# Kernel tuning notes

Hardware: AMD Instinct MI355X
Metric: run time of the kernel (lower is better)

The kernel has to match this reference:

```python
import jax, jax.numpy as jnp
import numpy as np

T, NC, NQ = 16, 32, 32
H, W, C = 128, 128, 1
DW, DR, DZ = 256, 256, 128
LABEL_DIM, Y_DIM = 2, 2
NHEADS = 8
NFEAT = int(DW * np.log(DW))  # performer default nb_features = int(d*ln d) = 1419


def setup_inputs() -> dict:
    key = jax.random.key(0)
    ks = iter(jax.random.split(key, 48))
    def nrm(shape, scale=0.02):
        return jax.random.normal(next(ks), shape, dtype=jnp.float32) * scale
    z = lambda *s: jnp.zeros(s, jnp.float32)
    return {
        'batch_train_images': jax.random.normal(next(ks), (T, NC, C, H, W), jnp.float32),
        'label_train': jax.random.normal(next(ks), (T, NC, LABEL_DIM), jnp.float32),
        'batch_test_images': jax.random.normal(next(ks), (T, NQ, C, H, W), jnp.float32),
        'conv1_w': nrm((32, C, 3, 3), 0.1), 'conv1_b': z(32),
        'conv2_w': nrm((48, 32, 3, 3), 0.05), 'conv2_b': z(48),
        'conv3_w': nrm((64, 48, 3, 3), 0.05), 'conv3_b': z(64),
        'enc_lw': nrm((DW, 4096)), 'enc_lb': z(DW),
        'ty_w': nrm((DW // 4, LABEL_DIM)), 'ty_b': z(DW // 4),
        'er_w1': nrm((DR, DW + DW // 4), 0.05), 'er_b1': z(DR),
        'er_w2': nrm((DR, DR), 0.05), 'er_b2': z(DR),
        'er_w3': nrm((DR, DR), 0.05), 'er_b3': z(DR),
        'wq': nrm((NHEADS, DW, DW), 0.05), 'wq_b': z(NHEADS, DW),
        'wk': nrm((NHEADS, DW, DW), 0.05), 'wk_b': z(NHEADS, DW),
        'wv': nrm((NHEADS, DW, DW), 0.05), 'wv_b': z(NHEADS, DW),
        'wo_w': nrm((DW, NHEADS * DW), 0.02), 'wo_b': z(DW),
        'rz_w': nrm((DZ, DR), 0.05), 'rz_b': z(DZ),
        'd0_w1': nrm((100, DW + DZ), 0.05), 'd0_b1': z(100),
        'd0_w2': nrm((100, 100), 0.05), 'd0_b2': z(100),
        'd0_w3': nrm((Y_DIM, 100), 0.05), 'd0_b3': z(Y_DIM),
        'proj': jax.random.normal(next(ks), (NFEAT, DW), jnp.float32),
    }


def _conv(x, w, b, stride):
    y = jax.lax.conv_general_dilated(x, w, (stride, stride), [(1, 1), (1, 1)],
                                     dimension_numbers=('NCHW', 'OIHW', 'NCHW'))
    return y + b[None, :, None, None]


def _maxpool2(x):
    return jax.lax.reduce_window(x, -jnp.inf, jax.lax.max, (1, 1, 2, 2), (1, 1, 2, 2), 'VALID')


def _encode(x, c1w, c1b, c2w, c2b, c3w, c3b, lw, lb):
    # BBBEncoder (mean weights): 128->64->32->pool16->8, 64ch, flatten 4096 -> DW
    x = jax.nn.relu(_conv(x, c1w, c1b, 2))
    x = jax.nn.relu(_conv(x, c2w, c2b, 2))
    x = _maxpool2(x)
    x = jax.nn.relu(_conv(x, c3w, c3b, 2))
    x = x.reshape(x.shape[0], -1)  # [B, 4096], NCHW order matches torch view
    return x @ lw.T + lb


def _softmax_kernel(x, proj, is_query):
    # performer softmax-kernel random features
    dn = x.shape[-1] ** -0.25
    ratio = proj.shape[0] ** -0.5
    xn = x * dn
    xd = jnp.einsum('bhnd,fd->bhnf', xn, proj)
    diag = 0.5 * jnp.sum(xn * xn, axis=-1, keepdims=True)
    if is_query:
        m = jnp.max(xd, axis=-1, keepdims=True)
    else:
        m = jnp.max(xd, axis=(-1, -2), keepdims=True)
    return ratio * (jnp.exp(xd - diag - jax.lax.stop_gradient(m)) + 1e-4)


def _forward(batch_train_images, label_train, batch_test_images,
             conv1_w, conv1_b, conv2_w, conv2_b, conv3_w, conv3_b, enc_lw, enc_lb,
             ty_w, ty_b, er_w1, er_b1, er_w2, er_b2, er_w3, er_b3,
             wq, wq_b, wk, wk_b, wv, wv_b, wo_w, wo_b, rz_w, rz_b,
             d0_w1, d0_b1, d0_w2, d0_b2, d0_w3, d0_b3, proj):
    enc = lambda im: _encode(im, conv1_w, conv1_b, conv2_w, conv2_b, conv3_w, conv3_b, enc_lw, enc_lb)
    x_qry = enc(batch_test_images.reshape(-1, C, H, W)).reshape(T, NQ, DW)
    x_ctx = enc(batch_train_images.reshape(-1, C, H, W)).reshape(T, NC, DW)
    ly = label_train @ ty_w.T + ty_b
    x = jnp.concatenate([x_ctx, ly], axis=2)  # [T, NC, DW + DW//4]
    h = jax.nn.relu(x @ er_w1.T + er_b1)
    h = jax.nn.relu(h @ er_w2.T + er_b2)
    rs = h @ er_w3.T + er_b3  # [T, NC, DR]
    # per-head projections (batched over the 8 heads)
    k_all = jnp.einsum('bnd,hed->bhne', x_ctx, wk) + wk_b[None, :, None, :]
    v_all = jnp.einsum('bnd,hed->bhne', rs, wv) + wv_b[None, :, None, :]
    q_all = jnp.einsum('bnd,hed->bhne', x_qry, wq) + wq_b[None, :, None, :]
    qp = _softmax_kernel(q_all, proj, True)   # [T, H, NQ, F]
    kp = _softmax_kernel(k_all, proj, False)  # [T, H, NC, F]
    d_inv = 1.0 / jnp.einsum('bhnf,bhf->bhn', qp, kp.sum(axis=2))
    ctx_mat = jnp.einsum('bhnf,bhne->bhfe', kp, v_all)
    outs = jnp.einsum('bhnf,bhfe->bhne', qp, ctx_mat) * d_inv[..., None]
    outs = outs.transpose(0, 2, 3, 1).reshape(T, NQ, -1)  # permute(0,2,3,1).view
    rep = outs @ wo_w.T + wo_b
    zz = rep @ rz_w.T + rz_b  # [T, NQ, DZ]
    xz = jnp.concatenate([x_qry, zz], axis=-1)
    h = jax.nn.relu(xz @ d0_w1.T + d0_b1)
    h = jax.nn.relu(h @ d0_w2.T + d0_b2)
    return jnp.tanh(h @ d0_w3.T + d0_b3)  # pr_y_mu [T, NQ, Y_DIM]


def reference(batch_train_images, label_train, batch_test_images,
              conv1_w, conv1_b, conv2_w, conv2_b, conv3_w, conv3_b, enc_lw, enc_lb,
              ty_w, ty_b, er_w1, er_b1, er_w2, er_b2, er_w3, er_b3,
              wq, wq_b, wk, wk_b, wv, wv_b, wo_w, wo_b, rz_w, rz_b,
              d0_w1, d0_b1, d0_w2, d0_b2, d0_w3, d0_b3, proj):
    pr_y_mu = _forward(batch_train_images, label_train, batch_test_images,
                       conv1_w, conv1_b, conv2_w, conv2_b, conv3_w, conv3_b, enc_lw, enc_lb,
                       ty_w, ty_b, er_w1, er_b1, er_w2, er_b2, er_w3, er_b3,
                       wq, wq_b, wk, wk_b, wv, wv_b, wo_w, wo_b, rz_w, rz_b,
                       d0_w1, d0_b1, d0_w2, d0_b2, d0_w3, d0_b3, proj)
    kl = jnp.float32(0.0)  # deterministic (mean-weight) BBB encoder -> KL constant
    return (pr_y_mu, kl)
```

## Files before the change

### kernel.cpp

```cpp
#include <hip/hip_runtime.h>
#include <math.h>

#define F_FEAT 1419
static constexpr float DN    = 0.25f;

typedef short short8 __attribute__((ext_vector_type(8)));
typedef float f32x4  __attribute__((ext_vector_type(4)));

static constexpr long OFF_XDQ  = 0;
static constexpr long OFF_XDK  = 5812224;
static constexpr long U_WQH = 0;
static constexpr long U_WQL = 524288;
static constexpr long U_WKH = 1048576;
static constexpr long U_WKL = 1572864;
static constexpr long U_WVH = 2097152;
static constexpr long U_WVL = 2621440;
static constexpr long OFF_ENCT = 4000000;
static constexpr long OFF_REPT = 6200000;
static constexpr long U_PH  = 23248896;
static constexpr long U_PL  = 23625728;
static constexpr long U_XCH = 24002560;
static constexpr long U_XCL = 24264704;
static constexpr long U_RSH = 24526848;
static constexpr long U_RSL = 24657920;
static constexpr long U_C3H = 25165824;
static constexpr long U_C3L = 29360128;
static constexpr long U_WOH = 25165824;
static constexpr long U_WOL = 25690112;
static constexpr long BASE     = 16777216;
static constexpr long OFF_XCTX = BASE + 0;
static constexpr long OFF_XQRY = BASE + 131072;
static constexpr long OFF_XCAT = BASE + 262144;
static constexpr long OFF_H1   = BASE + 425984;
static constexpr long OFF_H2   = BASE + 557056;
static constexpr long OFF_RS   = BASE + 688128;
static constexpr long U_QH  = (BASE + 819200) * 2;
static constexpr long U_QL  = U_QH + 1048576;
static constexpr long U_KH  = (BASE + 1867776) * 2;
static constexpr long U_KL  = U_KH + 1048576;
static constexpr long OFF_VA   = BASE + 2916352;
static constexpr long OFF_AW1  = BASE + 3964928;
static constexpr long U_ELH = (BASE + 3977344) * 2;
static constexpr long U_ELL = U_ELH + 1048576;
static constexpr long U_REPH = U_ELH;
static constexpr long U_REPL = U_ELL;
static constexpr long OFF_REP  = BASE + 5025920;
static constexpr long OFF_XZ   = BASE + 5156992;
static constexpr long OFF_DH1  = BASE + 5353600;
static constexpr long OFF_DH2  = BASE + 5404800;
static constexpr long OFF_MD   = BASE + 5456000;
static constexpr long OFF_AW   = 22233216;
static constexpr long OFF_AW3  = 22240128;

__device__ inline unsigned short f2bf(float f) {
    unsigned int x = __float_as_uint(f);
    unsigned int r = x + 0x7fffu + ((x >> 16) & 1u);
    return (unsigned short)(r >> 16);
}
__device__ inline float bf2f(unsigned short h) {
    return __uint_as_float((unsigned int)h << 16);
}
__device__ inline unsigned int cvtpk(float a, float b) {
    unsigned int r;
    asm("v_cvt_pk_bf16_f32 %0, %1, %2" : "=v"(r) : "v"(a), "v"(b));
    return r;
}

static constexpr int NA1 = 13824;
static constexpr int NA2 = NA1 + 1024;
static constexpr int NA3 = NA2 + 73728;
static constexpr int NA4 = NA3 + 1048576;

__global__ void k_wprepA(const float* __restrict__ w2, const float* __restrict__ w1,
                         const float* __restrict__ w3, const float* __restrict__ elw,
                         unsigned short* __restrict__ Aw, unsigned short* __restrict__ Aw1,
                         unsigned short* __restrict__ Aw3,
                         unsigned short* __restrict__ ELh, unsigned short* __restrict__ ELl)
{
    int i = blockIdx.x * 256 + threadIdx.x;
    if (i < NA1) {
        int ic  = i & 31;
        int m16 = (i >> 5) & 15;
        int emt = i >> 9;
        int mt  = emt % 3, e = emt / 3;
        Aw[i] = f2bf(w2[((mt * 16 + m16) * 32 + ic) * 9 + e]);
    } else if (i < NA2) {
        int j = i - NA1;
        int k = j & 31, m = (j >> 5) & 15, mt = j >> 9;
        Aw1[j] = (k < 9) ? f2bf(w1[(mt * 16 + m) * 9 + k]) : (unsigned short)0;
    } else if (i < NA3) {
        int j = i - NA2;
        int k  = j & 63;
        int m  = (j >> 6) & 15;
        int hl = (j >> 10) & 1;
        int mt = (j >> 11) & 3;
        int e  = j >> 13;
        unsigned short v = 0;
        if (k < 48) {
            float w = w3[((mt * 16 + m) * 48 + k) * 9 + e];
            unsigned short hi = f2bf(w);
            v = hl == 0 ? hi : f2bf(w - bf2f(hi));
        }
        Aw3[j] = v;
    } else if (i < NA4) {
        int j = i - NA3;
        float v = elw[j];
        unsigned short h = f2bf(v);
        ELh[j] = h; ELl[j] = f2bf(v - bf2f(h));
    }
}

static constexpr int NB1 = 376832;
static constexpr int NB2 = NB1 + 1572864;

__global__ void k_wprepB(const float* __restrict__ proj,
                         const float* __restrict__ wq, const float* __restrict__ wk,
                         const float* __restrict__ wv,
                         unsigned short* __restrict__ Ph, unsigned short* __restrict__ Pl,
                         unsigned short* __restrict__ Wqkv)
{
    int i = blockIdx.x * 256 + threadIdx.x;
    if (i < NB1) {
        float v = (i < 363264) ? proj[i] : 0.f;
        unsigned short h = f2bf(v);
        Ph[i] = h; Pl[i] = f2bf(v - bf2f(h));
    } else if (i < NB2) {
        int j = i - NB1;
        int y = j / 524288, jj = j % 524288;
        const float* s = (y == 0) ? wq : (y == 1) ? wk : wv;
        float v = s[jj];
        unsigned short h = f2bf(v);
        Wqkv[(long)y * 1048576 + jj] = h;
        Wqkv[(long)y * 1048576 + 524288 + jj] = f2bf(v - bf2f(h));
    }
}

#define TP 136
__launch_bounds__(256)
__global__ void k_conv12m(const float* __restrict__ train, const float* __restrict__ test,
                          const float* __restrict__ b1,
                          const unsigned short* __restrict__ Aw,
                          const unsigned short* __restrict__ Aw1,
                          const float* __restrict__ b2,
                          unsigned short* __restrict__ pool_out)
{
    const int g   = blockIdx.x;
    const int img = blockIdx.y;
    const float* in = (img < 512) ? (train + (long)img * 16384)
                                  : (test  + (long)(img - 512) * 16384);

    __shared__ unsigned short ring[9 * 66 * 40];
    __shared__ unsigned short tile[19 * TP];

    const int t = threadIdx.x;

    for (int i = t; i < 9 * 40; i += 256) {
        int sl = i / 40, icp = i % 40;
        ring[(sl * 66 + 0) * 40 + icp] = 0;
    }
    if (g == 0)
        for (int i = t; i < 66 * 40; i += 256) ring[i] = 0;
    if (t < 19) *(unsigned int*)&tile[t * TP + 2] = 0u;

    {
        const float4 z4 = make_float4(0.f, 0.f, 0.f, 0.f);
        for (int u = t; u < 19 * 32; u += 256) {
            int row = u >> 5, k = u & 31;
            int r2 = 16 * g - 3 + row;
            float4 v = (r2 >= 0) ? *(const float4*)(in + r2 * 128 + k * 4) : z4;
            uint2 d;
            d.x = cvtpk(v.x, v.y);
            d.y = cvtpk(v.z, v.w);
            *(uint2*)&tile[row * TP + 4 + k * 4] = d;
        }
    }
    __syncthreads();

    const int w    = t >> 6;
    const int lane = t & 63;
    const int cn   = lane & 15;
    const int quad = lane >> 4;

    short8 a1f0 = *(const short8*)&Aw1[(0 * 16 + cn) * 32 + quad * 8];
    short8 a1f1 = *(const short8*)&Aw1[(16 + cn) * 32 + quad * 8];
    float4 bsa = *(const float4*)&b1[quad * 4];
    float4 bsb = *(const float4*)&b1[16 + quad * 4];

    const int px2 = w * 16 + cn;
    const int tb  = 2 * px2 + 2;
    auto do_slice = [&](int sl) {
        const int rb = 2 * sl * TP + tb;
        uint4 pk = make_uint4(0u, 0u, 0u, 0u);
        if (quad == 0) {
            unsigned int w00 = *(const unsigned int*)&tile[rb];
            unsigned int w10 = *(const unsigned int*)&tile[rb + 2];
            unsigned int w01 = *(const unsigned int*)&tile[rb + TP];
            unsigned int w11 = *(const unsigned int*)&tile[rb + TP + 2];
            unsigned int w02 = *(const unsigned int*)&tile[rb + 2 * TP];
            unsigned int w12 = *(const unsigned int*)&tile[rb + 2 * TP + 2];
            pk.x = (w00 >> 16) | (w10 << 16);
            pk.y = (w10 >> 16) | (w01 & 0xffff0000u);
            pk.z = w11;
            pk.w = (w02 >> 16) | (w12 << 16);
        } else if (quad == 1) {
            pk.x = (*(const unsigned int*)&tile[rb + 2 * TP + 2]) >> 16;
        }
        short8 bfr = *(const short8*)&pk;
        f32x4 z = (f32x4){0.f, 0.f, 0.f, 0.f};
        f32x4 c0 = __builtin_amdgcn_mfma_f32_16x16x32_bf16(a1f0, bfr, z, 0, 0, 0);
        f32x4 c1 = __builtin_amdgcn_mfma_f32_16x16x32_bf16(a1f1, bfr, z, 0, 0, 0);
        uint2 u0, u1;
        u0.x = cvtpk(fmaxf(c0[0] + bsa.x, 0.f), fmaxf(c0[1] + bsa.y, 0.f));
        u0.y = cvtpk(fmaxf(c0[2] + bsa.z, 0.f), fmaxf(c0[3] + bsa.w, 0.f));
        u1.x = cvtpk(fmaxf(c1[0] + bsb.x, 0.f), fmaxf(c1[1] + bsb.y, 0.f));
        u1.y = cvtpk(fmaxf(c1[2] + bsb.z, 0.f), fmaxf(c1[3] + bsb.w, 0.f));
        *(uint2*)&ring[(sl * 66 + px2 + 1) * 40 + quad * 4]      = u0;
        *(uint2*)&ring[(sl * 66 + px2 + 1) * 40 + 16 + quad * 4] = u1;
    };
    if (g > 0) do_slice(0);
    #pragma unroll
    for (int sl = 1; sl < 9; sl++) do_slice(sl);

    short8 ca0 = *(const short8*)&Aw[((0 * 3 + 0) * 16 + cn) * 32 + quad * 8];
    short8 ca1 = *(const short8*)&Aw[((0 * 3 + 1) * 16 + cn) * 32 + quad * 8];
    short8 ca2 = *(const short8*)&Aw[((0 * 3 + 2) * 16 + cn) * 32 + quad * 8];
    __syncthreads();

    const int pr = w >> 1, xh = w & 1;
    f32x4 acc[3][2];
    #pragma unroll
    for (int mt = 0; mt < 3; mt++) {
        acc[mt][0] = (f32x4){0.f, 0.f, 0.f, 0.f};
        acc[mt][1] = (f32x4){0.f, 0.f, 0.f, 0.f};
    }

    #pragma unroll
    for (int e = 0; e < 9; e++) {
        int dy = e / 3, dx = e - 3 * dy;
        int c  = 2 * (xh * 16 + cn) + dx;
        int s0 = 4 * pr + dy;
        short8 b0  = *(const short8*)&ring[(s0 * 66 + c) * 40 + quad * 8];
        short8 b1f = *(const short8*)&ring[((s0 + 2) * 66 + c) * 40 + quad * 8];
        short8 na0, na1, na2;
        if (e < 8) {
            na0 = *(const short8*)&Aw[(((e + 1) * 3 + 0) * 16 + cn) * 32 + quad * 8];
            na1 = *(const short8*)&Aw[(((e + 1) * 3 + 1) * 16 + cn) * 32 + quad * 8];
            na2 = *(const short8*)&Aw[(((e + 1) * 3 + 2) * 16 + cn) * 32 + quad * 8];
        }
        acc[0][0] = __builtin_amdgcn_mfma_f32_16x16x32_bf16(ca0, b0,  acc[0][0], 0, 0, 0);
        acc[1][0] = __builtin_amdgcn_mfma_f32_16x16x32_bf16(ca1, b0,  acc[1][0], 0, 0, 0);
        acc[2][0] = __builtin_amdgcn_mfma_f32_16x16x32_bf16(ca2, b0,  acc[2][0], 0, 0, 0);
        acc[0][1] = __builtin_amdgcn_mfma_f32_16x16x32_bf16(ca0, b1f, acc[0][1], 0, 0, 0);
        acc[1][1] = __builtin_amdgcn_mfma_f32_16x16x32_bf16(ca1, b1f, acc[1][1], 0, 0, 0);
        acc[2][1] = __builtin_amdgcn_mfma_f32_16x16x32_bf16(ca2, b1f, acc[2][1], 0, 0, 0);
        if (e < 8) { ca0 = na0; ca1 = na1; ca2 = na2; }
    }

    {
        const int prow = 2 * g + pr;
        const int ppx  = xh * 8 + (cn >> 1);
        unsigned short* pb = pool_out + ((long)img * 256 + prow * 16 + ppx) * 96
                           + ((cn & 1) ? 48 : 0);
        #pragma unroll
        for (int mt = 0; mt < 3; mt++) {
            float4 bv = *(const float4*)&b2[mt * 16 + quad * 4];
            float m0, m1, m2, m3;
            {
                float v;
                v = fmaxf(fmaxf(acc[mt][0][0] + bv.x, acc[mt][1][0] + bv.x), 0.f);
                m0 = fmaxf(v, __shfl_xor(v, 1));
                v = fmaxf(fmaxf(acc[mt][0][1] + bv.y, acc[mt][1][1] + bv.y), 0.f);
                m1 = fmaxf(v, __shfl_xor(v, 1));
                v = fmaxf(fmaxf(acc[mt][0][2] + bv.z, acc[mt][1][2] + bv.z), 0.f);
                m2 = fmaxf(v, __shfl_xor(v, 1));
                v = fmaxf(fmaxf(acc[mt][0][3] + bv.w, acc[mt][1][3] + bv.w), 0.f);
                m3 = fmaxf(v, __shfl_xor(v, 1));
            }
            uint2 hv;
            hv.x = cvtpk(m0, m1);
            hv.y = cvtpk(m2, m3);
            uint2 sv = hv;
            if (cn & 1) {
                float d0 = m0 - bf2f((unsigned short)(hv.x & 0xffffu));
                float d1 = m1 - bf2f((unsigned short)(hv.x >> 16));
                float d2 = m2 - bf2f((unsigned short)(hv.y & 0xffffu));
                float d3 = m3 - bf2f((unsigned short)(hv.y >> 16));
                sv.x = cvtpk(d0, d1);
                sv.y = cvtpk(d2, d3);
            }
            *(uint2*)&pb[mt * 16 + quad * 4] = sv;
        }
    }
}

#define C3PITCH 104
__launch_bounds__(512)
__global__ void k_conv3m(const unsigned short* __restrict__ pool,
                         const unsigned short* __restrict__ Aw3,
                         const float* __restrict__ b3,
                         unsigned short* __restrict__ C3h, unsigned short* __restrict__ C3l)
{
    const int img = blockIdx.x;
    __shared__ unsigned short s_in[30120];
    const int t = threadIdx.x;

    uint4* s4 = (uint4*)s_in;
    const uint4 zz = make_uint4(0, 0, 0, 0);
    for (int i = t; i < 3765; i += 512) s4[i] = zz;
    __syncthreads();
    {
        int p = t >> 1, half = t & 1;
        const uint4* src = (const uint4*)(pool + ((long)img * 256 + p) * 96 + half * 48);
        int r = p >> 4, c = p & 15;
        uint4* dst = (uint4*)(s_in + ((r + 1) * 17 + (c + 1)) * C3PITCH + half * 48);
        #pragma unroll
        for (int j = 0; j < 6; j++) dst[j] = src[j];
    }
    __syncthreads();

    const int w = t >> 6, lane = t & 63;
    const int n = lane & 15, quad = lane >> 4;
    const int mt = w >> 1, ntb = (w & 1) * 2;

    f32x4 acc[2];
    acc[0] = (f32x4){0.f, 0.f, 0.f, 0.f};
    acc[1] = (f32x4){0.f, 0.f, 0.f, 0.f};

    for (int e = 0; e < 9; e++) {
        int dy = e / 3, dx = e - 3 * dy;
        const unsigned short* A0 = Aw3 + (long)(((e * 4 + mt) * 2 + 0) * 16 + n) * 64 + quad * 8;
        const unsigned short* A1 = Aw3 + (long)(((e * 4 + mt) * 2 + 1) * 16 + n) * 64 + quad * 8;
        short8 ah0 = *(const short8*)(A0);
        short8 ah1 = *(const short8*)(A0 + 32);
        short8 al0 = *(const short8*)(A1);
        short8 al1 = *(const short8*)(A1 + 32);
        #pragma unroll
        for (int j = 0; j < 2; j++) {
            int p = (ntb + j) * 16 + n;
            int y = p >> 3, x = p & 7;
            const unsigned short* Bp = s_in + ((2 * y + dy) * 17 + (2 * x + dx)) * C3PITCH + quad * 8;
            short8 bh0 = *(const short8*)(Bp);
            short8 bh1 = *(const short8*)(Bp + 32);
            short8 bl0 = *(const short8*)(Bp + 48);
            short8 bl1 = *(const short8*)(Bp + 48 + 32);
            acc[j] = __builtin_amdgcn_mfma_f32_16x16x32_bf16(ah0, bh0, acc[j], 0, 0, 0);
            acc[j] = __builtin_amdgcn_mfma_f32_16x16x32_bf16(ah1, bh1, acc[j], 0, 0, 0);
            acc[j] = __builtin_amdgcn_mfma_f32_16x16x32_bf16(ah0, bl0, acc[j], 0, 0, 0);
            acc[j] = __builtin_amdgcn_mfma_f32_16x16x32_bf16(ah1, bl1, acc[j], 0, 0, 0);
            acc[j] = __builtin_amdgcn_mfma_f32_16x16x32_bf16(al0, bh0, acc[j], 0, 0, 0);
            acc[j] = __builtin_amdgcn_mfma_f32_16x16x32_bf16(al1, bh1, acc[j], 0, 0, 0);
        }
    }

    unsigned short* oh = C3h + (long)img * 4096;
    unsigned short* ol = C3l + (long)img * 4096;
    #pragma unroll
    for (int reg = 0; reg < 4; reg++) {
        int oc = mt * 16 + quad * 4 + reg;
        float bias = b3[oc];
        #pragma unroll
        for (int j = 0; j < 2; j++) {
            int p = (ntb + j) * 16 + n;
            float v = fmaxf(acc[j][reg] + bias, 0.f);
            unsigned short h = f2bf(v);
            oh[oc * 64 + p] = h;
            ol[oc * 64 + p] = f2bf(v - bf2f(h));
        }
    }
}

template<int OUTMODE>
__launch_bounds__(256)
__global__ void mgemm(const unsigned short* __restrict__ Xh0, const unsigned short* __restrict__ Xl0,
                      const unsigned short* __restrict__ Wph, const unsigned short* __restrict__ Wpl,
                      const float* __restrict__ Bb, float* __restrict__ Yf,
                      unsigned short* __restrict__ Yh, unsigned short* __restrict__ Yl,
                      int M, int N, int K, int ldY, float scale,
                      long sX, long sW, long sB, long sY, int kChunk)
{
    const int z = blockIdx.z;
    const unsigned short* Xh = Xh0 + (OUTMODE == 3 ? 0 : (long)z * sX);
    const unsigned short* Xl = Xl0 + (OUTMODE == 3 ? 0 : (long)z * sX);
    const unsigned short* Wh = Wph + (OUTMODE == 3 ? 0 : (long)z * sW);
    const unsigned short* Wl = Wpl + (OUTMODE == 3 ? 0 : (long)z * sW);
    const float* B = Bb ? (Bb + (OUTMODE == 3 ? 0 : (long)z * sB)) : nullptr;
    int k0 = 0, k1 = K;
    if (OUTMODE == 3) { k0 = z * kChunk; k1 = min(K, k0 + kChunk); }

    __shared__ unsigned short sAh[64 * 40], sAl[64 * 40], sBh[64 * 40], sBl[64 * 40];

    const int t = threadIdx.x;
    const int m0 = blockIdx.y * 64, n0 = blockIdx.x * 64;
    const int r = t >> 2, kq = (t & 3) * 8;

    const int w = t >> 6, lane = t & 63;
    const int wm = (w & 1) * 32, wn = (w >> 1) * 32;
    const int cn = lane & 15, quad = lane >> 4;

    f32x4 acc[2][2];
    acc[0][0] = acc[0][1] = acc[1][0] = acc[1][1] = (f32x4){0.f, 0.f, 0.f, 0.f};

    for (int kb = k0; kb < k1; kb += 32) {
        *(uint4*)&sAh[r * 40 + kq] = *(const uint4*)&Xh[(long)(m0 + r) * K + kb + kq];
        *(uint4*)&sAl[r * 40 + kq] = *(const uint4*)&Xl[(long)(m0 + r) * K + kb + kq];
        *(uint4*)&sBh[r * 40 + kq] = *(const uint4*)&Wh[(long)(n0 + r) * K + kb + kq];
        *(uint4*)&sBl[r * 40 + kq] = *(const uint4*)&Wl[(long)(n0 + r) * K + kb + kq];
        __syncthreads();
        short8 axh[2], axl[2], bxh[2], bxl[2];
        #pragma unroll
        for (int i = 0; i < 2; i++) {
            axh[i] = *(const short8*)&sAh[(wm + i * 16 + cn) * 40 + quad * 8];
            axl[i] = *(const short8*)&sAl[(wm + i * 16 + cn) * 40 + quad * 8];
            bxh[i] = *(const short8*)&sBh[(wn + i * 16 + cn) * 40 + quad * 8];
            bxl[i] = *(const short8*)&sBl[(wn + i * 16 + cn) * 40 + quad * 8];
        }
        #pragma unroll
        for (int i = 0; i < 2; i++)
            #pragma unroll
            for (int j = 0; j < 2; j++) {
                acc[i][j] = __builtin_amdgcn_mfma_f32_16x16x32_bf16(axh[i], bxh[j], acc[i][j], 0, 0, 0);
                acc[i][j] = __builtin_amdgcn_mfma_f32_16x16x32_bf16(axh[i], bxl[j], acc[i][j], 0, 0, 0);
                acc[i][j] = __builtin_amdgcn_mfma_f32_16x16x32_bf16(axl[i], bxh[j], acc[i][j], 0, 0, 0);
            }
        __syncthreads();
    }

    #pragma unroll
    for (int i = 0; i < 2; i++) {
        #pragma unroll
        for (int reg = 0; reg < 4; reg++) {
            int row = m0 + wm + i * 16 + quad * 4 + reg;
            #pragma unroll
            for (int j = 0; j < 2; j++) {
                int col = n0 + wn + j * 16 + cn;
                if (col >= N) continue;
                float v = acc[i][j][reg] * scale;
                if (OUTMODE == 3) {
                    (Yf + (long)z * sY)[(long)row * ldY + col] = v;
                } else if (OUTMODE == 0) {
                    if (B) v += B[col];
                    (Yf + (long)z * sY)[(long)row * ldY + col] = v;
                } else {
                    if (B) v += B[col];
                    unsigned short h = f2bf(v);
                    (Yh + (long)z * sY)[(long)row * ldY + col] = h;
                    (Yl + (long)z * sY)[(long)row * ldY + col] = f2bf(v - bf2f(h));
                }
            }
        }
    }
}

__global__ void k_red_enc(const float* __restrict__ tmp, const float* __restrict__ elb,
                          float* __restrict__ x_ctx, unsigned short* __restrict__ XCh,
                          unsigned short* __restrict__ XCl, float* __restrict__ xcat,
                          const float* __restrict__ label, const float* __restrict__ tyw,
                          const float* __restrict__ tyb,
                          const float* __restrict__ wow, unsigned short* __restrict__ WOh,
                          unsigned short* __restrict__ WOl)
{
    int b = blockIdx.x;
    int tt = threadIdx.x;
    if (b < 1024) {
        int i = b * 256 + tt;
        int r = i >> 8, c = i & 255;
        float v = elb[c];
        #pragma unroll
        for (int z = 0; z < 8; z++) v += tmp[(long)z * 262144 + i];
        x_ctx[i] = v;
        unsigned short h = f2bf(v);
        XCh[i] = h; XCl[i] = f2bf(v - bf2f(h));
        if (r < 512) xcat[r * 320 + c] = v;
    } else if (b < 1152) {
        int i = (b - 1024) * 256 + tt;
        int r = i >> 6, e = i & 63;
        xcat[r * 320 + 256 + e] = tyb[e] + label[r * 2] * tyw[e * 2] + label[r * 2 + 1] * tyw[e * 2 + 1];
    } else {
        int i = (b - 1152) * 256 + tt;
        float v = wow[i];
        unsigned short h = f2bf(v);
        WOh[i] = h; WOl[i] = f2bf(v - bf2f(h));
    }
}

__global__ void k_red_rep(const float* __restrict__ tmp, const float* __restrict__ wob,
                          float* __restrict__ rep,
                          const float* __restrict__ xq, float* __restrict__ xz)
{
    int b = blockIdx.x;
    int tt = threadIdx.x;
    if (b < 512) {
        int i = b * 256 + tt;
        int c = i & 255;
        float v = wob[c];
        #pragma unroll
        for (int z = 0; z < 4; z++) v += tmp[(long)z * 131072 + i];
        rep[i] = v;
    } else {
        int i = (b - 512) * 256 + tt;
        int r = i >> 8, c = i & 255;
        xz[r * 384 + c] = xq[i];
    }
}

template<int BM, int BN, int BK, int ACT, bool FIN, bool WP>
__launch_bounds__(256)
__global__ void gemm_k(const float* __restrict__ X, const float* __restrict__ W,
                       const float* __restrict__ B, float* __restrict__ Y,
                       int M, int N, int K, int ldY,
                       unsigned short* __restrict__ Ph2, unsigned short* __restrict__ Pl2)
{
    __shared__ float As[BK][BM + 4];
    __shared__ float Bs[BK][BN + 4];
    const int t = threadIdx.x;
    const int tx = t & 15, ty = t >> 4;
    const int m0 = blockIdx.y * BM, n0 = blockIdx.x * BN;
    float acc[2][2] = {{0.f, 0.f}, {0.f, 0.f}};

    for (int kb = 0; kb < K; kb += BK) {
        for (int i = t; i < BM * BK; i += 256) {
            int rr = i / BK, c = i % BK;
            int mm = m0 + rr, kk = kb + c;
            As[c][rr] = (mm < M && kk < K) ? X[(long)mm * K + kk] : 0.f;
        }
        for (int i = t; i < BN * BK; i += 256) {
            int rr = i / BK, c = i % BK;
            int nn = n0 + rr, kk = kb + c;
            Bs[c][rr] = (nn < N && kk < K) ? W[(long)nn * K + kk] : 0.f;
        }
        __syncthreads();
        #pragma unroll
        for (int kk = 0; kk < BK; kk++) {
            float2 a2 = *(const float2*)&As[kk][ty * 2];
            float2 b2 = *(const float2*)&Bs[kk][tx * 2];
            acc[0][0] += a2.x * b2.x; acc[0][1] += a2.x * b2.y;
            acc[1][0] += a2.y * b2.x; acc[1][1] += a2.y * b2.y;
        }
        __syncthreads();
    }

    #pragma unroll
    for (int i = 0; i < 2; i++) {
        int mm = m0 + ty * 2 + i;
        if (mm >= M) continue;
        #pragma unroll
        for (int j = 0; j < 2; j++) {
            int nn = n0 + tx * 2 + j;
            if (nn >= N) continue;
            float v = acc[i][j] + (B ? B[nn] : 0.f);
            if (ACT == 1) v = fmaxf(v, 0.f);
            if (ACT == 2) v = tanhf(v);
            Y[(long)mm * ldY + nn] = v;
            if (WP) {
                unsigned short h = f2bf(v);
                Ph2[(long)mm * ldY + nn] = h;
                Pl2[(long)mm * ldY + nn] = f2bf(v - bf2f(h));
            }
        }
    }
    if (FIN && t == 0 && blockIdx.x == 0 && blockIdx.y == 0) Y[1024] = 0.f;
}

__launch_bounds__(256)
__global__ void k_maxdiag(const float* __restrict__ xdq, const float* __restrict__ xdk,
                          const unsigned short* __restrict__ Qh, const unsigned short* __restrict__ Ql,
                          const unsigned short* __restrict__ Kh, const unsigned short* __restrict__ Kl,
                          float* __restrict__ dq, float* __restrict__ mq,
                          float* __restrict__ dk, float* __restrict__ mk)
{
    __shared__ float red[8];
    const int bx = blockIdx.x;
    const int t = threadIdx.x;

    if (bx < 4096) {
        const int tok = bx;
        float v = bf2f(Qh[(long)tok * 256 + t]) + bf2f(Ql[(long)tok * 256 + t]);
        float s = v * v;
        for (int d = 1; d < 64; d <<= 1) s += __shfl_xor(s, d);
        if ((t & 63) == 0) red[t >> 6] = s;

        float m = -1e30f;
        #pragma unroll
        for (int j = 0; j < 6; j++) {
            int f = t + j * 256;
            if (f < F_FEAT) m = fmaxf(m, xdq[(long)tok * F_FEAT + f]);
        }
        for (int d = 1; d < 64; d <<= 1) m = fmaxf(m, __shfl_xor(m, d));
        if ((t & 63) == 0) red[4 + (t >> 6)] = m;
        __syncthreads();
        if (t == 0) {
            dq[tok] = (red[0] + red[1] + red[2] + red[3]) * (1.f / 32.f);
            mq[tok] = fmaxf(fmaxf(red[4], red[5]), fmaxf(red[6], red[7]));
        }
    } else {
        const int kb = bx - 4096;
        const long tok0 = (long)kb * 32;
        const int row = t >> 3, j = t & 7;

        float s = 0.f;
        const unsigned short* ph = Kh + (tok0 + row) * 256 + j * 32;
        const unsigned short* pl = Kl + (tok0 + row) * 256 + j * 32;
        for (int q = 0; q < 32; q++) { float v = bf2f(ph[q]) + bf2f(pl[q]); s += v * v; }
        s += __shfl_xor(s, 1); s += __shfl_xor(s, 2); s += __shfl_xor(s, 4);
        if (j == 0) dk[tok0 + row] = s * (1.f / 32.f);

        const float* base = xdk + tok0 * F_FEAT;
        float m = -1e30f;
        for (int i = t; i < 32 * F_FEAT; i += 256) m = fmaxf(m, base[i]);
        for (int d = 1; d < 64; d <<= 1) m = fmaxf(m, __shfl_xor(m, d));
        if ((t & 63) == 0) red[t >> 6] = m;
        __syncthreads();
        if (t == 0) mk[kb] = fmaxf(fmaxf(red[0], red[1]), fmaxf(red[2], red[3]));
    }
}

__launch_bounds__(256)
__global__ void k_attn(const float* __restrict__ qp, const float* __restrict__ kp,
                       const float* __restrict__ va,
                       const float* __restrict__ dq, const float* __restrict__ mq,
                       const float* __restrict__ dk, const float* __restrict__ mk,
                       unsigned short* __restrict__ REPh, unsigned short* __restrict__ REPl)
{
    const int tt = blockIdx.x;
    const int h  = blockIdx.y;
    const long row0 = ((long)h * 16 + tt) * 32;
    const int kb = h * 16 + tt;

    __shared__ float s_q[32][68];
    __shared__ float s_k[32][68];
    __shared__ float s_A[32][33];
    __shared__ float s_di[32];
    __shared__ float s_v[32 * 256];
    __shared__ float s_cq[32], s_ck[32];

    const int t = threadIdx.x;
    const int n = t >> 3;
    const int mq_ = (t & 7) * 4;

    if (t < 32) {
        s_cq[t] = dq[row0 + t] + mq[row0 + t];
        s_ck[t] = dk[row0 + t] + mk[kb];
    }
    __syncthreads();

    float acc[4] = {0, 0, 0, 0};
    for (int fc = 0; fc < F_FEAT; fc += 64) {
        for (int i = t; i < 2048; i += 256) {
            int rr = i >> 6, ff = i & 63;
            int fg = fc + ff;
            if (fg < F_FEAT) {
                s_q[rr][ff] = expf(qp[(row0 + rr) * F_FEAT + fg] - s_cq[rr]) + 1e-4f;
                s_k[rr][ff] = expf(kp[(row0 + rr) * F_FEAT + fg] - s_ck[rr]) + 1e-4f;
            } else {
                s_q[rr][ff] = 0.f;
                s_k[rr][ff] = 0.f;
            }
        }
        __syncthreads();
        #pragma unroll 8
        for (int ff = 0; ff < 64; ff++) {
            float a = s_q[n][ff];
            #pragma unroll
            for (int j = 0; j < 4; j++) acc[j] += a * s_k[mq_ + j][ff];
        }
        __syncthreads();
    }

    float rsum = acc[0] + acc[1] + acc[2] + acc[3];
    rsum += __shfl_xor(rsum, 1);
    rsum += __shfl_xor(rsum, 2);
    rsum += __shfl_xor(rsum, 4);
    #pragma unroll
    for (int j = 0; j < 4; j++) s_A[n][mq_ + j] = acc[j];
    if ((t & 7) == 0) s_di[n] = 1.f / rsum;
    for (int i = t; i < 8192; i += 256) s_v[i] = va[row0 * 256 + i];
    __syncthreads();

    const int e0 = t & 7;
    float out[32];
    #pragma unroll
    for (int j = 0; j < 32; j++) out[j] = 0.f;
    for (int m = 0; m < 32; m++) {
        float a = s_A[n][m];
        #pragma unroll
        for (int j = 0; j < 32; j++) out[j] += a * s_v[m * 256 + e0 + 8 * j];
    }
    float di = s_di[n];
    unsigned short* dsth = REPh + ((long)tt * 32 + n) * 2048;
    unsigned short* dstl = REPl + ((long)tt * 32 + n) * 2048;
    #pragma unroll
    for (int j = 0; j < 32; j++) {
        int e = e0 + 8 * j;
        float val = out[j] * di;
        unsigned short hh = f2bf(val);
        dsth[e * 8 + h] = hh;
        dstl[e * 8 + h] = f2bf(val - bf2f(hh));
    }
}

extern "C" void kernel_launch(void* const* d_in, const int* in_sizes, int n_in,
                              void* d_out, int out_size, void* d_ws, size_t ws_size,
                              hipStream_t stream)
{
    const float* train  = (const float*)d_in[0];
    const float* label  = (const float*)d_in[1];
    const float* test   = (const float*)d_in[2];
    const float* c1w = (const float*)d_in[3];  const float* c1b = (const float*)d_in[4];
    const float* c2w = (const float*)d_in[5];  const float* c2b = (const float*)d_in[6];
    const float* c3w = (const float*)d_in[7];  const float* c3b = (const float*)d_in[8];
    const float* elw = (const float*)d_in[9];  const float* elb = (const float*)d_in[10];
    const float* tyw = (const float*)d_in[11]; const float* tyb = (const float*)d_in[12];
    const float* ew1 = (const float*)d_in[13]; const float* eb1 = (const float*)d_in[14];
    const float* ew2 = (const float*)d_in[15]; const float* eb2 = (const float*)d_in[16];
    const float* ew3 = (const float*)d_in[17]; const float* eb3 = (const float*)d_in[18];
    const float* wq  = (const float*)d_in[19]; const float* wqb = (const float*)d_in[20];
    const float* wk  = (const float*)d_in[21]; const float* wkb = (const float*)d_in[22];
    const float* wv  = (const float*)d_in[23]; const float* wvb = (const float*)d_in[24];
    const float* wow = (const float*)d_in[25]; const float* wob = (const float*)d_in[26];
    const float* rzw = (const float*)d_in[27]; const float* rzb = (const float*)d_in[28];
    const float* dw1 = (const float*)d_in[29]; const float* db1 = (const float*)d_in[30];
    const float* dw2 = (const float*)d_in[31]; const float* db2 = (const float*)d_in[32];
    const float* dw3 = (const float*)d_in[33]; const float* db3 = (const float*)d_in[34];
    const float* proj= (const float*)d_in[35];

    float* wsf = (float*)d_ws;
    unsigned short* usw = (unsigned short*)d_ws;
    float* out = (float*)d_out;

    unsigned short* A_pool = usw;
    float* x_ctx  = wsf + OFF_XCTX;
    float* x_qry  = wsf + OFF_XQRY;
    float* xcat   = wsf + OFF_XCAT;
    float* h1     = wsf + OFF_H1;
    float* h2     = wsf + OFF_H2;
    float* rs     = wsf + OFF_RS;
    float* v_all  = wsf + OFF_VA;
    float* rep    = wsf + OFF_REP;
    float* xz     = wsf + OFF_XZ;
    float* dh1    = wsf + OFF_DH1;
    float* dh2    = wsf + OFF_DH2;
    float* xd_q   = wsf + OFF_XDQ;
    float* xd_k   = wsf + OFF_XDK;
    float* enc_t  = wsf + OFF_ENCT;
    float* rep_t  = wsf + OFF_REPT;
    float* dqv    = wsf + OFF_MD;
    float* mqv    = wsf + OFF_MD + 4096;
    float* dkv    = wsf + OFF_MD + 8192;
    float* mkv    = wsf + OFF_MD + 12288;
    unsigned short* Aw  = (unsigned short*)(wsf + OFF_AW);
    unsigned short* Aw3 = (unsigned short*)(wsf + OFF_AW3);
    unsigned short* Aw1 = (unsigned short*)(wsf + OFF_AW1);

    unsigned short* Wqkv = usw + U_WQH;
    unsigned short* WQh = usw + U_WQH; unsigned short* WQl = usw + U_WQL;
    unsigned short* WKh = usw + U_WKH; unsigned short* WKl = usw + U_WKL;
    unsigned short* WVh = usw + U_WVH; unsigned short* WVl = usw + U_WVL;
    unsigned short* Ph  = usw + U_PH;  unsigned short* Pl  = usw + U_PL;
    unsigned short* XCh = usw + U_XCH; unsigned short* XCl = usw + U_XCL;
    unsigned short* RSh = usw + U_RSH; unsigned short* RSl = usw + U_RSL;
    unsigned short* C3h = usw + U_C3H; unsigned short* C3l = usw + U_C3L;
    unsigned short* Qh  = usw + U_QH;  unsigned short* Ql  = usw + U_QL;
    unsigned short* Kh  = usw + U_KH;  unsigned short* Kl  = usw + U_KL;
    unsigned short* ELh = usw + U_ELH; unsigned short* ELl = usw + U_ELL;
    unsigned short* WOh = usw + U_WOH; unsigned short* WOl = usw + U_WOL;
    unsigned short* REPh= usw + U_REPH;unsigned short* REPl= usw + U_REPL;

    k_wprepA<<<4442, 256, 0, stream>>>(c2w, c1w, c3w, elw, Aw, Aw1, Aw3, ELh, ELl);

    k_conv12m<<<dim3(8, 1024), 256, 0, stream>>>(train, test, c1b, Aw, Aw1, c2b, A_pool);
    k_conv3m<<<1024, 512, 0, stream>>>(A_pool, Aw3, c3b, C3h, C3l);

    k_wprepB<<<7616, 256, 0, stream>>>(proj, wq, wk, wv, Ph, Pl, Wqkv);

    mgemm<3><<<dim3(4, 16, 8), 256, 0, stream>>>(
        C3h, C3l, ELh, ELl, nullptr, enc_t, nullptr, nullptr,
        1024, 256, 4096, 256, 1.f, 0, 0, 0, 262144, 512);
    k_red_enc<<<3200, 256, 0, stream>>>(enc_t, elb, x_ctx, XCh, XCl, xcat,
                                        label, tyw, tyb, wow, WOh, WOl);

    gemm_k<32,32,32,1,false,false><<<dim3(8, 16), 256, 0, stream>>>(xcat, ew1, eb1, h1, 512, 256, 320, 256, nullptr, nullptr);
    gemm_k<32,32,32,1,false,false><<<dim3(8, 16), 256, 0, stream>>>(h1, ew2, eb2, h2, 512, 256, 256, 256, nullptr, nullptr);
    gemm_k<32,32,32,0,false,true ><<<dim3(8, 16), 256, 0, stream>>>(h2, ew3, eb3, rs, 512, 256, 256, 256, RSh, RSl);

    mgemm<1><<<dim3(4, 8, 8), 256, 0, stream>>>(
        XCh + 512 * 256, XCl + 512 * 256, WQh, WQl, wqb, nullptr, Qh, Ql,
        512, 256, 256, 256, 1.f, 0, 65536, 256, 131072, 0);
    mgemm<1><<<dim3(4, 8, 8), 256, 0, stream>>>(
        XCh, XCl, WKh, WKl, wkb, nullptr, Kh, Kl,
        512, 256, 256, 256, 1.f, 0, 65536, 256, 131072, 0);
    mgemm<0><<<dim3(4, 8, 8), 256, 0, stream>>>(
        RSh, RSl, WVh, WVl, wvb, v_all, nullptr, nullptr,
        512, 256, 256, 256, 1.f, 0, 65536, 256, 131072, 0);

    mgemm<0><<<dim3(23, 64, 2), 256, 0, stream>>>(
        Qh, Ql, Ph, Pl, nullptr, xd_q, nullptr, nullptr,
        4096, F_FEAT, 256, F_FEAT, DN, 2097152, 0, 0, 5812224, 0);

    k_maxdiag<<<4224, 256, 0, stream>>>(xd_q, xd_k, Qh, Ql, Kh, Kl, dqv, mqv, dkv, mkv);

    k_attn<<<dim3(16, 8), 256, 0, stream>>>(xd_q, xd_k, v_all, dqv, mqv, dkv, mkv, REPh, REPl);

    mgemm<3><<<dim3(4, 8, 4), 256, 0, stream>>>(
        REPh, REPl, WOh, WOl, nullptr, rep_t, nullptr, nullptr,
        512, 256, 2048, 256, 1.f, 0, 0, 0, 131072, 512);
    k_red_rep<<<1024, 256, 0, stream>>>(rep_t, wob, rep, x_qry, xz);

    gemm_k<32,32,32,0,false,false><<<dim3(4, 16), 256, 0, stream>>>(rep, rzw, rzb, xz + 256, 512, 128, 256, 384, nullptr, nullptr);

    gemm_k<32,32,32,1,false,false><<<dim3(4, 16), 256, 0, stream>>>(xz, dw1, db1, dh1, 512, 100, 384, 100, nullptr, nullptr);
    gemm_k<32,32,32,1,false,false><<<dim3(4, 16), 256, 0, stream>>>(dh1, dw2, db2, dh2, 512, 100, 100, 100, nullptr, nullptr);
    gemm_k<32,32,32,2,true ,false><<<dim3(1, 16), 256, 0, stream>>>(dh2, dw3, db3, out, 512, 2, 100, 2, nullptr, nullptr);
}
```

Before: 771.8 us.

## Split performer attention into feature-split partial scores and column-split output kernel

The single attention kernel, which ran only 128 blocks, becomes two kernels. The first splits the 1419 random features into four chunks per block group and writes partial 32x32 score tiles to workspace. The second sums the partials, normalises, and computes the output over four 64-column slices of V. This raises block count to fill the GPU and pads shared rows to 65 to avoid bank conflicts, at the cost of an extra launch and a small partial-sum round trip through global memory.

```diff
diff --git a/kernel.cpp b/kernel.cpp
--- a/kernel.cpp
+++ b/kernel.cpp
@@ -17,6 +17,7 @@
 static constexpr long U_WVL = 2621440;
 static constexpr long OFF_ENCT = 4000000;
 static constexpr long OFF_REPT = 6200000;
+static constexpr long OFF_PA   = 11624448;
 static constexpr long U_PH  = 23248896;
 static constexpr long U_PL  = 23625728;
 static constexpr long U_XCH = 24002560;
@@ -614,23 +615,22 @@
     }
 }
 
+#define NSPLIT 4
+#define FCH 355
 __launch_bounds__(256)
-__global__ void k_attn(const float* __restrict__ qp, const float* __restrict__ kp,
-                       const float* __restrict__ va,
-                       const float* __restrict__ dq, const float* __restrict__ mq,
-                       const float* __restrict__ dk, const float* __restrict__ mk,
-                       unsigned short* __restrict__ REPh, unsigned short* __restrict__ REPl)
-{
-    const int tt = blockIdx.x;
-    const int h  = blockIdx.y;
-    const long row0 = ((long)h * 16 + tt) * 32;
-    const int kb = h * 16 + tt;
-
-    __shared__ float s_q[32][68];
-    __shared__ float s_k[32][68];
-    __shared__ float s_A[32][33];
-    __shared__ float s_di[32];
-    __shared__ float s_v[32 * 256];
+__global__ void k_attn1(const float* __restrict__ qp, const float* __restrict__ kp,
+                        const float* __restrict__ dq, const float* __restrict__ mq,
+                        const float* __restrict__ dk, const float* __restrict__ mk,
+                        float* __restrict__ pA)
+{
+    const int s  = blockIdx.x;
+    const int kb = blockIdx.y;
+    const long row0 = (long)kb * 32;
+    const int f0 = s * FCH;
+    const int f1 = min(F_FEAT, f0 + FCH);
+
+    __shared__ float s_q[32 * 65];
+    __shared__ float s_k[32 * 65];
     __shared__ float s_cq[32], s_ck[32];
 
     const int t = threadIdx.x;
@@ -643,54 +643,89 @@
     }
     __syncthreads();
 
-    float acc[4] = {0, 0, 0, 0};
-    for (int fc = 0; fc < F_FEAT; fc += 64) {
+    float acc[4] = {0.f, 0.f, 0.f, 0.f};
+    for (int fc = f0; fc < f1; fc += 64) {
         for (int i = t; i < 2048; i += 256) {
             int rr = i >> 6, ff = i & 63;
             int fg = fc + ff;
-            if (fg < F_FEAT) {
-                s_q[rr][ff] = expf(qp[(row0 + rr) * F_FEAT + fg] - s_cq[rr]) + 1e-4f;
-                s_k[rr][ff] = expf(kp[(row0 + rr) * F_FEAT + fg] - s_ck[rr]) + 1e-4f;
-            } else {
-                s_q[rr][ff] = 0.f;
-                s_k[rr][ff] = 0.f;
+            float qv = 0.f, kv = 0.f;
+            if (fg < f1) {
+                qv = expf(qp[(row0 + rr) * F_FEAT + fg] - s_cq[rr]) + 1e-4f;
+                kv = expf(kp[(row0 + rr) * F_FEAT + fg] - s_ck[rr]) + 1e-4f;
             }
+            s_q[rr * 65 + ff] = qv;
+            s_k[rr * 65 + ff] = kv;
         }
         __syncthreads();
         #pragma unroll 8
         for (int ff = 0; ff < 64; ff++) {
-            float a = s_q[n][ff];
+            float a = s_q[n * 65 + ff];
             #pragma unroll
-            for (int j = 0; j < 4; j++) acc[j] += a * s_k[mq_ + j][ff];
+            for (int j = 0; j < 4; j++) acc[j] += a * s_k[(mq_ + j) * 65 + ff];
         }
         __syncthreads();
     }
 
-    float rsum = acc[0] + acc[1] + acc[2] + acc[3];
-    rsum += __shfl_xor(rsum, 1);
-    rsum += __shfl_xor(rsum, 2);
-    rsum += __shfl_xor(rsum, 4);
+    float* dst = pA + ((long)kb * NSPLIT + s) * 1024;
     #pragma unroll
-    for (int j = 0; j < 4; j++) s_A[n][mq_ + j] = acc[j];
-    if ((t & 7) == 0) s_di[n] = 1.f / rsum;
-    for (int i = t; i < 8192; i += 256) s_v[i] = va[row0 * 256 + i];
+    for (int j = 0; j < 4; j++) dst[n * 32 + mq_ + j] = acc[j];
+}
+
+__launch_bounds__(256)
+__global__ void k_attn2(const float* __restrict__ pA, const float* __restrict__ va,
+                        unsigned short* __restrict__ REPh, unsigned short* __restrict__ REPl)
+{
+    const int ec = blockIdx.x;
+    const int kb = blockIdx.y;
+    const int h = kb >> 4, tt = kb & 15;
+    const long row0 = (long)kb * 32;
+
+    __shared__ float s_A[32][33];
+    __shared__ float s_di[32];
+    __shared__ float s_v[32 * 64];
+
+    const int t = threadIdx.x;
+
+    {
+        const float* base = pA + (long)kb * NSPLIT * 1024 + t * 4;
+        float4 v0 = *(const float4*)(base);
+        float4 v1 = *(const float4*)(base + 1024);
+        float4 v2 = *(const float4*)(base + 2048);
+        float4 v3 = *(const float4*)(base + 3072);
+        int r = t >> 3, c = (t & 7) * 4;
+        s_A[r][c]     = v0.x + v1.x + v2.x + v3.x;
+        s_A[r][c + 1] = v0.y + v1.y + v2.y + v3.y;
+        s_A[r][c + 2] = v0.z + v1.z + v2.z + v3.z;
+        s_A[r][c + 3] = v0.w + v1.w + v2.w + v3.w;
+    }
+    for (int i = t; i < 2048; i += 256) {
+        int m = i >> 6, e = i & 63;
+        s_v[m * 64 + e] = va[row0 * 256 + m * 256 + ec * 64 + e];
+    }
     __syncthreads();
-
-    const int e0 = t & 7;
-    float out[32];
+    if (t < 32) {
+        float s = 0.f;
+        #pragma unroll
+        for (int m = 0; m < 32; m++) s += s_A[t][m];
+        s_di[t] = 1.f / s;
+    }
+    __syncthreads();
+
+    const int n = t >> 3, e0 = t & 7;
+    float out[8];
     #pragma unroll
-    for (int j = 0; j < 32; j++) out[j] = 0.f;
+    for (int j = 0; j < 8; j++) out[j] = 0.f;
     for (int m = 0; m < 32; m++) {
         float a = s_A[n][m];
         #pragma unroll
-        for (int j = 0; j < 32; j++) out[j] += a * s_v[m * 256 + e0 + 8 * j];
+        for (int j = 0; j < 8; j++) out[j] += a * s_v[m * 64 + e0 + 8 * j];
     }
     float di = s_di[n];
     unsigned short* dsth = REPh + ((long)tt * 32 + n) * 2048;
     unsigned short* dstl = REPl + ((long)tt * 32 + n) * 2048;
     #pragma unroll
-    for (int j = 0; j < 32; j++) {
-        int e = e0 + 8 * j;
+    for (int j = 0; j < 8; j++) {
+        int e = ec * 64 + e0 + 8 * j;
         float val = out[j] * di;
         unsigned short hh = f2bf(val);
         dsth[e * 8 + h] = hh;
@@ -743,6 +778,7 @@
     float* xd_k   = wsf + OFF_XDK;
     float* enc_t  = wsf + OFF_ENCT;
     float* rep_t  = wsf + OFF_REPT;
+    float* pA     = wsf + OFF_PA;
     float* dqv    = wsf + OFF_MD;
     float* mqv    = wsf + OFF_MD + 4096;
     float* dkv    = wsf + OFF_MD + 8192;
@@ -798,7 +834,8 @@
 
     k_maxdiag<<<4224, 256, 0, stream>>>(xd_q, xd_k, Qh, Ql, Kh, Kl, dqv, mqv, dkv, mkv);
 
-    k_attn<<<dim3(16, 8), 256, 0, stream>>>(xd_q, xd_k, v_all, dqv, mqv, dkv, mkv, REPh, REPl);
+    k_attn1<<<dim3(NSPLIT, 128), 256, 0, stream>>>(xd_q, xd_k, dqv, mqv, dkv, mkv, pA);
+    k_attn2<<<dim3(4, 128), 256, 0, stream>>>(pA, v_all, REPh, REPl);
 
     mgemm<3><<<dim3(4, 8, 4), 256, 0, stream>>>(
         REPh, REPl, WOh, WOl, nullptr, rep_t, nullptr, nullptr,
```

After: 698.1 us. -9.5%, faster.
